# Performance work log

Measured on AMD Instinct MI355X. Metric: run time of the kernel, lower is better.

## Reference

```python
import jax, jax.numpy as jnp
import numpy as np

B, S, D, H = 4, 2048, 1024, 16
HD = D // H
MASKED_BIAS = -10000.0

def setup_inputs() -> dict:
    key = jax.random.key(0)
    ks = jax.random.split(key, 10)
    s = 0.02
    return {
        "hidden_states": jax.random.normal(ks[0], (B, S, D), dtype=jnp.float32),
        "Wq": jax.random.normal(ks[1], (D, D), dtype=jnp.float32) * s,
        "bq": jax.random.normal(ks[2], (D,), dtype=jnp.float32) * s,
        "Wk": jax.random.normal(ks[3], (D, D), dtype=jnp.float32) * s,
        "bk": jax.random.normal(ks[4], (D,), dtype=jnp.float32) * s,
        "Wv": jax.random.normal(ks[5], (D, D), dtype=jnp.float32) * s,
        "bv": jax.random.normal(ks[6], (D,), dtype=jnp.float32) * s,
        "Wo": jax.random.normal(ks[7], (D, D), dtype=jnp.float32) * s,
        "bo": jax.random.normal(ks[8], (D,), dtype=jnp.float32) * s,
        "comp": jnp.zeros((D,), dtype=jnp.float32),
    }

def reference(hidden_states, Wq, bq, Wk, bk, Wv, bv, Wo, bo, comp):
    x = hidden_states
    # torch Linear: y = x @ W.T + b
    q = (x @ Wq.T + bq).reshape(B, S, H, HD).transpose(0, 2, 1, 3)  # [B,H,S,hd]
    k = (x @ Wk.T + bk).reshape(B, S, H, HD).transpose(0, 2, 1, 3)
    v = (x @ Wv.T + bv).reshape(B, S, H, HD).transpose(0, 2, 1, 3)
    scores = jnp.einsum('bhqd,bhkd->bhqk', q, k) / jnp.sqrt(jnp.asarray(HD, dtype=q.dtype))
    causal = jnp.tril(jnp.ones((S, S), dtype=bool))  # [S,S]
    scores = jnp.where(causal[None, None], scores, jnp.asarray(MASKED_BIAS, dtype=scores.dtype))
    attn = jax.nn.softmax(scores, axis=-1)  # dropout p=0 (eval)
    out = jnp.einsum('bhqk,bhkd->bhqd', attn, v)  # [B,H,S,hd]
    out = out.transpose(0, 2, 1, 3).reshape(B, S, D)
    out = out @ Wo.T + bo
    out = out + comp[None, None, :]
    return out
```

## Files before the change

### kernel.cpp

```cpp
#include <hip/hip_runtime.h>
#include <hip/hip_bf16.h>

#define NB 4
#define NS 2048
#define ND 1024
#define NH 16
#define NHD 64
#define NM (NB*NS)

typedef __bf16 bf16_t;
typedef bf16_t bf8  __attribute__((ext_vector_type(8)));
typedef bf16_t bf4v __attribute__((ext_vector_type(4)));
typedef float  f4   __attribute__((ext_vector_type(4)));

#define GLDS16(g, l) __builtin_amdgcn_global_load_lds( \
    (const __attribute__((address_space(1))) void*)(g), \
    (__attribute__((address_space(3))) void*)(l), 16, 0, 0)

__global__ __launch_bounds__(256) void cvt_all(const float* __restrict__ x,
                                               const float* __restrict__ wq,
                                               const float* __restrict__ wk,
                                               const float* __restrict__ wv,
                                               const float* __restrict__ wo,
                                               bf16_t* __restrict__ Xb,
                                               bf16_t* __restrict__ Wqkv,
                                               bf16_t* __restrict__ Wob) {
    const int i = blockIdx.x * 256 + threadIdx.x;
    const float* src;
    bf16_t* dst;
    int off;
    if (i < 2097152) {
        src = x; dst = Xb; off = i;
    } else {
        const int j = i - 2097152;
        const int w = j >> 18;
        off = j & 262143;
        src = (w == 0 ? wq : w == 1 ? wk : w == 2 ? wv : wo);
        dst = (w == 3 ? Wob : Wqkv + ((size_t)w << 20));
    }
    const float4 v = ((const float4*)src)[off];
    bf4v o;
    o[0] = (bf16_t)v.x; o[1] = (bf16_t)v.y; o[2] = (bf16_t)v.z; o[3] = (bf16_t)v.w;
    ((bf4v*)dst)[off] = o;
}

__global__ __launch_bounds__(256) void gemm_qkv(const bf16_t* __restrict__ A,
                                                const bf16_t* __restrict__ Bw,
                                                const float* __restrict__ bq,
                                                const float* __restrict__ bk,
                                                const float* __restrict__ bv,
                                                bf16_t* __restrict__ Qh,
                                                bf16_t* __restrict__ Kh,
                                                bf16_t* __restrict__ VTh) {
    __shared__ __align__(16) bf16_t As[128 * 32];
    __shared__ __align__(16) bf16_t Bs[128 * 32];
    const int t = threadIdx.x;
    const int wave = t >> 6, lane = t & 63, ln = lane & 15, quad = lane >> 4;
    const int wm = (wave >> 1) * 64, wn = (wave & 1) * 64;
    const int m0 = blockIdx.y * 128, n0 = blockIdx.x * 128;
    const int K = 1024;

    f4 acc[4][4];
    const f4 z = {0.f, 0.f, 0.f, 0.f};
#pragma unroll
    for (int i = 0; i < 4; ++i)
#pragma unroll
        for (int j = 0; j < 4; ++j) acc[i][j] = z;

    const int srow = wave * 16 + (lane >> 2);
    const int scol = (lane & 3) * 8;
    const bf16_t* Ag0 = A  + (size_t)(m0 + srow) * K + scol;
    const bf16_t* Ag1 = A  + (size_t)(m0 + srow + 64) * K + scol;
    const bf16_t* Bg0 = Bw + (size_t)(n0 + srow) * K + scol;
    const bf16_t* Bg1 = Bw + (size_t)(n0 + srow + 64) * K + scol;
    bf16_t* Al0 = &As[srow * 32 + scol];
    bf16_t* Al1 = &As[(srow + 64) * 32 + scol];
    bf16_t* Bl0 = &Bs[srow * 32 + scol];
    bf16_t* Bl1 = &Bs[(srow + 64) * 32 + scol];

    for (int k0 = 0; k0 < K; k0 += 32) {
        __syncthreads();
        GLDS16(Ag0 + k0, Al0);
        GLDS16(Ag1 + k0, Al1);
        GLDS16(Bg0 + k0, Bl0);
        GLDS16(Bg1 + k0, Bl1);
        __syncthreads();
        bf8 af[4], bfr[4];
#pragma unroll
        for (int mt = 0; mt < 4; ++mt) af[mt]  = *(const bf8*)(&As[(wm + mt * 16 + ln) * 32 + quad * 8]);
#pragma unroll
        for (int nt = 0; nt < 4; ++nt) bfr[nt] = *(const bf8*)(&Bs[(wn + nt * 16 + ln) * 32 + quad * 8]);
#pragma unroll
        for (int mt = 0; mt < 4; ++mt)
#pragma unroll
            for (int nt = 0; nt < 4; ++nt)
                acc[mt][nt] = __builtin_amdgcn_mfma_f32_16x16x32_bf16(af[mt], bfr[nt], acc[mt][nt], 0, 0, 0);
    }

    const int sec = n0 >> 10;
#pragma unroll
    for (int nt = 0; nt < 4; ++nt) {
        const int gn = n0 + wn + nt * 16 + ln;
        const int nn = gn & 1023;
        const int hh = nn >> 6, d = nn & 63;
        const float bias = (sec == 0 ? bq[nn] : (sec == 1 ? bk[nn] : bv[nn]));
        if (sec < 2) {
            bf16_t* dstBase = (sec == 0 ? Qh : Kh);
#pragma unroll
            for (int mt = 0; mt < 4; ++mt) {
#pragma unroll
                for (int r = 0; r < 4; ++r) {
                    const int gm = m0 + wm + mt * 16 + quad * 4 + r;
                    const int b = gm >> 11, s = gm & 2047;
                    dstBase[((size_t)(b * NH + hh) * NS + s) * NHD + d] = (bf16_t)(acc[mt][nt][r] + bias);
                }
            }
        } else {
#pragma unroll
            for (int mt = 0; mt < 4; ++mt) {
                const int gm0 = m0 + wm + mt * 16 + quad * 4;
                const int b = gm0 >> 11, s = gm0 & 2047;
                bf4v pk;
#pragma unroll
                for (int r = 0; r < 4; ++r) pk[r] = (bf16_t)(acc[mt][nt][r] + bias);
                *(bf4v*)(&VTh[((size_t)(b * NH + hh) * NHD + d) * NS + s]) = pk;
            }
        }
    }
}

__global__ __launch_bounds__(256) void attn_kernel(const bf16_t* __restrict__ Q,
                                                   const bf16_t* __restrict__ K,
                                                   const bf16_t* __restrict__ VT,
                                                   bf16_t* __restrict__ O) {
    __shared__ __align__(16) bf16_t Ks[64 * 72];
    __shared__ __align__(16) bf16_t Vt[64 * 72];
    const int L = blockIdx.x;
    const int mm = L >> 3;
    const int h  = ((mm >> 5) << 3) | (L & 7);
    const int qt = 31 - (mm & 31);
    const int q0 = qt * 64;
    const int jmax = qt;
    const size_t head_off = (size_t)h * NS * NHD;
    const int t = threadIdx.x;
    const int wave = t >> 6, lane = t & 63, ln = lane & 15, quad = lane >> 4;

    const bf16_t* Qrow = Q + head_off + (size_t)(q0 + wave * 16 + ln) * NHD;
    bf8 qf0 = *(const bf8*)(Qrow + quad * 8);
    bf8 qf1 = *(const bf8*)(Qrow + 32 + quad * 8);
#pragma unroll
    for (int e = 0; e < 8; ++e) {
        qf0[e] = (bf16_t)((float)qf0[e] * 0.125f);
        qf1[e] = (bf16_t)((float)qf1[e] * 0.125f);
    }

    const bf16_t* Kg  = K  + head_off;
    const bf16_t* VTg = VT + head_off;
    const int krow0 = t >> 3, kcol = (t & 7) * 8;

    uint4 kr0 = *(const uint4*)(Kg + (size_t)krow0 * NHD + kcol);
    uint4 kr1 = *(const uint4*)(Kg + (size_t)(krow0 + 32) * NHD + kcol);
    uint4 vr0 = *(const uint4*)(VTg + (size_t)krow0 * NS + kcol);
    uint4 vr1 = *(const uint4*)(VTg + (size_t)(krow0 + 32) * NS + kcol);
    *(uint4*)(&Ks[krow0 * 72 + kcol])        = kr0;
    *(uint4*)(&Ks[(krow0 + 32) * 72 + kcol]) = kr1;
    *(uint4*)(&Vt[krow0 * 72 + kcol])        = vr0;
    *(uint4*)(&Vt[(krow0 + 32) * 72 + kcol]) = vr1;
    __syncthreads();

    f4 o[4];
    const f4 z = {0.f, 0.f, 0.f, 0.f};
#pragma unroll
    for (int i = 0; i < 4; ++i) o[i] = z;
    float ls = 0.f;

#pragma unroll 1
    for (int j = 0; j <= jmax; ++j) {
        if (j < jmax) {
            const size_t nb = (size_t)(j + 1) * 64;
            kr0 = *(const uint4*)(Kg + (nb + krow0) * NHD + kcol);
            kr1 = *(const uint4*)(Kg + (nb + krow0 + 32) * NHD + kcol);
            vr0 = *(const uint4*)(VTg + (size_t)krow0 * NS + nb + kcol);
            vr1 = *(const uint4*)(VTg + (size_t)(krow0 + 32) * NS + nb + kcol);
        }

        f4 s[4];
        __builtin_amdgcn_s_setprio(1);
#pragma unroll
        for (int nt = 0; nt < 4; ++nt) {
            const bf8 kf0 = *(const bf8*)(&Ks[(nt * 16 + ln) * 72 + quad * 8]);
            const bf8 kf1 = *(const bf8*)(&Ks[(nt * 16 + ln) * 72 + 32 + quad * 8]);
            s[nt] = z;
            s[nt] = __builtin_amdgcn_mfma_f32_16x16x32_bf16(kf0, qf0, s[nt], 0, 0, 0);
            s[nt] = __builtin_amdgcn_mfma_f32_16x16x32_bf16(kf1, qf1, s[nt], 0, 0, 0);
        }
        __builtin_amdgcn_s_setprio(0);

        if (j == jmax) {
            const int kv0 = j * 64;
            const int rowq = q0 + wave * 16 + ln;
#pragma unroll
            for (int nt = 0; nt < 4; ++nt) {
#pragma unroll
                for (int r = 0; r < 4; ++r)
                    if (kv0 + nt * 16 + quad * 4 + r > rowq) s[nt][r] = -1e30f;
            }
        }

#pragma unroll
        for (int nt = 0; nt < 4; ++nt)
#pragma unroll
            for (int r = 0; r < 4; ++r) {
                const float p = __expf(s[nt][r]);
                s[nt][r] = p;
                ls += p;
            }

        unsigned int w[4][2];
#pragma unroll
        for (int nt = 0; nt < 4; ++nt)
#pragma unroll
            for (int rr = 0; rr < 2; ++rr) {
                union { bf16_t hx[2]; unsigned int u; } u;
                u.hx[0] = (bf16_t)s[nt][2 * rr];
                u.hx[1] = (bf16_t)s[nt][2 * rr + 1];
                w[nt][rr] = u.u;
            }
        union Frag { unsigned int d[4]; bf8 v; } f0, f1;
        {
            unsigned int a, b;
            a = w[0][0]; b = w[1][0];
            asm volatile("v_permlane32_swap_b32 %0, %1" : "+v"(a), "+v"(b));
            asm volatile("v_permlane16_swap_b32 %0, %1" : "+v"(a), "+v"(b));
            f0.d[0] = a; f0.d[2] = b;
            a = w[0][1]; b = w[1][1];
            asm volatile("v_permlane32_swap_b32 %0, %1" : "+v"(a), "+v"(b));
            asm volatile("v_permlane16_swap_b32 %0, %1" : "+v"(a), "+v"(b));
            f0.d[1] = a; f0.d[3] = b;
            a = w[2][0]; b = w[3][0];
            asm volatile("v_permlane32_swap_b32 %0, %1" : "+v"(a), "+v"(b));
            asm volatile("v_permlane16_swap_b32 %0, %1" : "+v"(a), "+v"(b));
            f1.d[0] = a; f1.d[2] = b;
            a = w[2][1]; b = w[3][1];
            asm volatile("v_permlane32_swap_b32 %0, %1" : "+v"(a), "+v"(b));
            asm volatile("v_permlane16_swap_b32 %0, %1" : "+v"(a), "+v"(b));
            f1.d[1] = a; f1.d[3] = b;
        }
        const bf8 p0 = f0.v;
        const bf8 p1 = f1.v;

        __builtin_amdgcn_s_setprio(1);
#pragma unroll
        for (int dt = 0; dt < 4; ++dt) {
            const bf8 v0 = *(const bf8*)(&Vt[(dt * 16 + ln) * 72 + quad * 8]);
            const bf8 v1 = *(const bf8*)(&Vt[(dt * 16 + ln) * 72 + 32 + quad * 8]);
            o[dt] = __builtin_amdgcn_mfma_f32_16x16x32_bf16(p0, v0, o[dt], 0, 0, 0);
            o[dt] = __builtin_amdgcn_mfma_f32_16x16x32_bf16(p1, v1, o[dt], 0, 0, 0);
        }
        __builtin_amdgcn_s_setprio(0);

        if (j < jmax) {
            __syncthreads();
            *(uint4*)(&Ks[krow0 * 72 + kcol])        = kr0;
            *(uint4*)(&Ks[(krow0 + 32) * 72 + kcol]) = kr1;
            *(uint4*)(&Vt[krow0 * 72 + kcol])        = vr0;
            *(uint4*)(&Vt[(krow0 + 32) * 72 + kcol]) = vr1;
            __syncthreads();
        }
    }

    ls += __shfl_xor(ls, 16);
    ls += __shfl_xor(ls, 32);

    const int b = h >> 4, hh = h & 15;
#pragma unroll
    for (int r = 0; r < 4; ++r) {
        const float inv = 1.f / __shfl(ls, quad * 4 + r);
        const int gs = q0 + wave * 16 + quad * 4 + r;
#pragma unroll
        for (int dt = 0; dt < 4; ++dt)
            O[((size_t)(b * NS + gs)) * ND + hh * NHD + dt * 16 + ln] = (bf16_t)(o[dt][r] * inv);
    }
}

__global__ __launch_bounds__(256) void gemm_proj(const bf16_t* __restrict__ A,
                                                 const bf16_t* __restrict__ Bw,
                                                 const float* __restrict__ bo,
                                                 const float* __restrict__ comp,
                                                 float* __restrict__ out) {
    __shared__ __align__(16) bf16_t As[128 * 32];
    __shared__ __align__(16) bf16_t Bs[128 * 32];
    const int t = threadIdx.x;
    const int wave = t >> 6, lane = t & 63, ln = lane & 15, quad = lane >> 4;
    const int wm = (wave >> 1) * 64, wn = (wave & 1) * 64;
    const int nwg = gridDim.x * gridDim.y;
    int flat = blockIdx.y * gridDim.x + blockIdx.x;
    flat = (flat & 7) * (nwg >> 3) + (flat >> 3);
    const int m0 = (flat / gridDim.x) * 128, n0 = (flat % gridDim.x) * 128;
    const int K = 1024;

    f4 acc[4][4];
    const f4 z = {0.f, 0.f, 0.f, 0.f};
#pragma unroll
    for (int i = 0; i < 4; ++i)
#pragma unroll
        for (int j = 0; j < 4; ++j) acc[i][j] = z;

    const int srow = wave * 16 + (lane >> 2);
    const int scol = (lane & 3) * 8;
    const bf16_t* Ag0 = A  + (size_t)(m0 + srow) * K + scol;
    const bf16_t* Ag1 = A  + (size_t)(m0 + srow + 64) * K + scol;
    const bf16_t* Bg0 = Bw + (size_t)(n0 + srow) * K + scol;
    const bf16_t* Bg1 = Bw + (size_t)(n0 + srow + 64) * K + scol;
    bf16_t* Al0 = &As[srow * 32 + scol];
    bf16_t* Al1 = &As[(srow + 64) * 32 + scol];
    bf16_t* Bl0 = &Bs[srow * 32 + scol];
    bf16_t* Bl1 = &Bs[(srow + 64) * 32 + scol];

    for (int k0 = 0; k0 < K; k0 += 32) {
        __syncthreads();
        GLDS16(Ag0 + k0, Al0);
        GLDS16(Ag1 + k0, Al1);
        GLDS16(Bg0 + k0, Bl0);
        GLDS16(Bg1 + k0, Bl1);
        __syncthreads();
        bf8 af[4], bfr[4];
#pragma unroll
        for (int mt = 0; mt < 4; ++mt) af[mt]  = *(const bf8*)(&As[(wm + mt * 16 + ln) * 32 + quad * 8]);
#pragma unroll
        for (int nt = 0; nt < 4; ++nt) bfr[nt] = *(const bf8*)(&Bs[(wn + nt * 16 + ln) * 32 + quad * 8]);
#pragma unroll
        for (int mt = 0; mt < 4; ++mt)
#pragma unroll
            for (int nt = 0; nt < 4; ++nt)
                acc[mt][nt] = __builtin_amdgcn_mfma_f32_16x16x32_bf16(bfr[nt], af[mt], acc[mt][nt], 0, 0, 0);
    }

#pragma unroll
    for (int nt = 0; nt < 4; ++nt) {
        const int gn = n0 + wn + nt * 16 + quad * 4;
        const float4 b4 = *(const float4*)(bo + gn);
        const float4 c4 = *(const float4*)(comp + gn);
#pragma unroll
        for (int mt = 0; mt < 4; ++mt) {
            const int gm = m0 + wm + mt * 16 + ln;
            float4 v;
            v.x = acc[mt][nt][0] + b4.x + c4.x;
            v.y = acc[mt][nt][1] + b4.y + c4.y;
            v.z = acc[mt][nt][2] + b4.z + c4.z;
            v.w = acc[mt][nt][3] + b4.w + c4.w;
            *(float4*)(&out[(size_t)gm * ND + gn]) = v;
        }
    }
}

extern "C" void kernel_launch(void* const* d_in, const int* in_sizes, int n_in,
                              void* d_out, int out_size, void* d_ws, size_t ws_size,
                              hipStream_t stream) {
    const float* x    = (const float*)d_in[0];
    const float* Wq   = (const float*)d_in[1];
    const float* bq   = (const float*)d_in[2];
    const float* Wk   = (const float*)d_in[3];
    const float* bk   = (const float*)d_in[4];
    const float* Wv   = (const float*)d_in[5];
    const float* bv   = (const float*)d_in[6];
    const float* Wo   = (const float*)d_in[7];
    const float* bo   = (const float*)d_in[8];
    const float* comp = (const float*)d_in[9];
    float* out = (float*)d_out;

    char* w = (char*)d_ws;
    bf16_t* Xb   = (bf16_t*)(w);
    bf16_t* Wqkv = (bf16_t*)(w + 16777216);
    bf16_t* Wob  = (bf16_t*)(w + 23068672);
    bf16_t* Qh   = (bf16_t*)(w + 25165824);
    bf16_t* Kh   = (bf16_t*)(w + 41943040);
    bf16_t* VTh  = (bf16_t*)(w + 58720256);
    bf16_t* AOb  = (bf16_t*)(w + 75497472);

    cvt_all<<<12288, 256, 0, stream>>>(x, Wq, Wk, Wv, Wo, Xb, Wqkv, Wob);
    gemm_qkv<<<dim3(3072 / 128, NM / 128), 256, 0, stream>>>(Xb, Wqkv, bq, bk, bv, Qh, Kh, VTh);
    attn_kernel<<<2048, 256, 0, stream>>>(Qh, Kh, VTh, AOb);
    gemm_proj<<<dim3(1024 / 128, NM / 128), 256, 0, stream>>>(AOb, Wob, bo, comp, out);
}
```

Before: 273.5 us.

## Double-buffer LDS tiles in GEMMs and attention, swizzle QKV block order

Adds two-stage LDS buffering to both GEMM kernels and the attention kernel. The next K-slice (or K/V tile) is now issued into the alternate buffer while MFMAs run on the current one, which cuts each iteration from two barriers to one. The QKV GEMM also gets an XCD-style block remap (stride 192) to improve L2 locality. The cost is double the LDS per block, which may lower occupancy. The GEMM path also relies on the global_load_lds writes having completed at the single trailing barrier.

```diff
diff --git a/kernel.cpp b/kernel.cpp
--- a/kernel.cpp
+++ b/kernel.cpp
@@ -52,12 +52,14 @@
                                                 bf16_t* __restrict__ Qh,
                                                 bf16_t* __restrict__ Kh,
                                                 bf16_t* __restrict__ VTh) {
-    __shared__ __align__(16) bf16_t As[128 * 32];
-    __shared__ __align__(16) bf16_t Bs[128 * 32];
+    __shared__ __align__(16) bf16_t As[2][128 * 32];
+    __shared__ __align__(16) bf16_t Bs[2][128 * 32];
     const int t = threadIdx.x;
     const int wave = t >> 6, lane = t & 63, ln = lane & 15, quad = lane >> 4;
     const int wm = (wave >> 1) * 64, wn = (wave & 1) * 64;
-    const int m0 = blockIdx.y * 128, n0 = blockIdx.x * 128;
+    int flat = blockIdx.y * gridDim.x + blockIdx.x;
+    flat = (flat & 7) * 192 + (flat >> 3);
+    const int m0 = (flat / gridDim.x) * 128, n0 = (flat % gridDim.x) * 128;
     const int K = 1024;
 
     f4 acc[4][4];
@@ -73,28 +75,34 @@
     const bf16_t* Ag1 = A  + (size_t)(m0 + srow + 64) * K + scol;
     const bf16_t* Bg0 = Bw + (size_t)(n0 + srow) * K + scol;
     const bf16_t* Bg1 = Bw + (size_t)(n0 + srow + 64) * K + scol;
-    bf16_t* Al0 = &As[srow * 32 + scol];
-    bf16_t* Al1 = &As[(srow + 64) * 32 + scol];
-    bf16_t* Bl0 = &Bs[srow * 32 + scol];
-    bf16_t* Bl1 = &Bs[(srow + 64) * 32 + scol];
-
+    const int so0 = srow * 32 + scol, so1 = (srow + 64) * 32 + scol;
+
+    GLDS16(Ag0, &As[0][so0]);
+    GLDS16(Ag1, &As[0][so1]);
+    GLDS16(Bg0, &Bs[0][so0]);
+    GLDS16(Bg1, &Bs[0][so1]);
+    __syncthreads();
+
+    int cur = 0;
     for (int k0 = 0; k0 < K; k0 += 32) {
-        __syncthreads();
-        GLDS16(Ag0 + k0, Al0);
-        GLDS16(Ag1 + k0, Al1);
-        GLDS16(Bg0 + k0, Bl0);
-        GLDS16(Bg1 + k0, Bl1);
-        __syncthreads();
+        if (k0 + 32 < K) {
+            GLDS16(Ag0 + k0 + 32, &As[cur ^ 1][so0]);
+            GLDS16(Ag1 + k0 + 32, &As[cur ^ 1][so1]);
+            GLDS16(Bg0 + k0 + 32, &Bs[cur ^ 1][so0]);
+            GLDS16(Bg1 + k0 + 32, &Bs[cur ^ 1][so1]);
+        }
         bf8 af[4], bfr[4];
 #pragma unroll
-        for (int mt = 0; mt < 4; ++mt) af[mt]  = *(const bf8*)(&As[(wm + mt * 16 + ln) * 32 + quad * 8]);
-#pragma unroll
-        for (int nt = 0; nt < 4; ++nt) bfr[nt] = *(const bf8*)(&Bs[(wn + nt * 16 + ln) * 32 + quad * 8]);
+        for (int mt = 0; mt < 4; ++mt) af[mt]  = *(const bf8*)(&As[cur][(wm + mt * 16 + ln) * 32 + quad * 8]);
+#pragma unroll
+        for (int nt = 0; nt < 4; ++nt) bfr[nt] = *(const bf8*)(&Bs[cur][(wn + nt * 16 + ln) * 32 + quad * 8]);
 #pragma unroll
         for (int mt = 0; mt < 4; ++mt)
 #pragma unroll
             for (int nt = 0; nt < 4; ++nt)
                 acc[mt][nt] = __builtin_amdgcn_mfma_f32_16x16x32_bf16(af[mt], bfr[nt], acc[mt][nt], 0, 0, 0);
+        __syncthreads();
+        cur ^= 1;
     }
 
     const int sec = n0 >> 10;
@@ -133,8 +141,8 @@
                                                    const bf16_t* __restrict__ K,
                                                    const bf16_t* __restrict__ VT,
                                                    bf16_t* __restrict__ O) {
-    __shared__ __align__(16) bf16_t Ks[64 * 72];
-    __shared__ __align__(16) bf16_t Vt[64 * 72];
+    __shared__ __align__(16) bf16_t Ks[2][64 * 72];
+    __shared__ __align__(16) bf16_t Vt[2][64 * 72];
     const int L = blockIdx.x;
     const int mm = L >> 3;
     const int h  = ((mm >> 5) << 3) | (L & 7);
@@ -162,10 +170,10 @@
     uint4 kr1 = *(const uint4*)(Kg + (size_t)(krow0 + 32) * NHD + kcol);
     uint4 vr0 = *(const uint4*)(VTg + (size_t)krow0 * NS + kcol);
     uint4 vr1 = *(const uint4*)(VTg + (size_t)(krow0 + 32) * NS + kcol);
-    *(uint4*)(&Ks[krow0 * 72 + kcol])        = kr0;
-    *(uint4*)(&Ks[(krow0 + 32) * 72 + kcol]) = kr1;
-    *(uint4*)(&Vt[krow0 * 72 + kcol])        = vr0;
-    *(uint4*)(&Vt[(krow0 + 32) * 72 + kcol]) = vr1;
+    *(uint4*)(&Ks[0][krow0 * 72 + kcol])        = kr0;
+    *(uint4*)(&Ks[0][(krow0 + 32) * 72 + kcol]) = kr1;
+    *(uint4*)(&Vt[0][krow0 * 72 + kcol])        = vr0;
+    *(uint4*)(&Vt[0][(krow0 + 32) * 72 + kcol]) = vr1;
     __syncthreads();
 
     f4 o[4];
@@ -176,6 +184,8 @@
 
 #pragma unroll 1
     for (int j = 0; j <= jmax; ++j) {
+        const bf16_t* KsB = &Ks[j & 1][0];
+        const bf16_t* VtB = &Vt[j & 1][0];
         if (j < jmax) {
             const size_t nb = (size_t)(j + 1) * 64;
             kr0 = *(const uint4*)(Kg + (nb + krow0) * NHD + kcol);
@@ -188,8 +198,8 @@
         __builtin_amdgcn_s_setprio(1);
 #pragma unroll
         for (int nt = 0; nt < 4; ++nt) {
-            const bf8 kf0 = *(const bf8*)(&Ks[(nt * 16 + ln) * 72 + quad * 8]);
-            const bf8 kf1 = *(const bf8*)(&Ks[(nt * 16 + ln) * 72 + 32 + quad * 8]);
+            const bf8 kf0 = *(const bf8*)(&KsB[(nt * 16 + ln) * 72 + quad * 8]);
+            const bf8 kf1 = *(const bf8*)(&KsB[(nt * 16 + ln) * 72 + 32 + quad * 8]);
             s[nt] = z;
             s[nt] = __builtin_amdgcn_mfma_f32_16x16x32_bf16(kf0, qf0, s[nt], 0, 0, 0);
             s[nt] = __builtin_amdgcn_mfma_f32_16x16x32_bf16(kf1, qf1, s[nt], 0, 0, 0);
@@ -252,21 +262,22 @@
         __builtin_amdgcn_s_setprio(1);
 #pragma unroll
         for (int dt = 0; dt < 4; ++dt) {
-            const bf8 v0 = *(const bf8*)(&Vt[(dt * 16 + ln) * 72 + quad * 8]);
-            const bf8 v1 = *(const bf8*)(&Vt[(dt * 16 + ln) * 72 + 32 + quad * 8]);
+            const bf8 v0 = *(const bf8*)(&VtB[(dt * 16 + ln) * 72 + quad * 8]);
+            const bf8 v1 = *(const bf8*)(&VtB[(dt * 16 + ln) * 72 + 32 + quad * 8]);
             o[dt] = __builtin_amdgcn_mfma_f32_16x16x32_bf16(p0, v0, o[dt], 0, 0, 0);
             o[dt] = __builtin_amdgcn_mfma_f32_16x16x32_bf16(p1, v1, o[dt], 0, 0, 0);
         }
         __builtin_amdgcn_s_setprio(0);
 
         if (j < jmax) {
-            __syncthreads();
-            *(uint4*)(&Ks[krow0 * 72 + kcol])        = kr0;
-            *(uint4*)(&Ks[(krow0 + 32) * 72 + kcol]) = kr1;
-            *(uint4*)(&Vt[krow0 * 72 + kcol])        = vr0;
-            *(uint4*)(&Vt[(krow0 + 32) * 72 + kcol]) = vr1;
-            __syncthreads();
-        }
+            bf16_t* KsN = &Ks[(j + 1) & 1][0];
+            bf16_t* VtN = &Vt[(j + 1) & 1][0];
+            *(uint4*)(&KsN[krow0 * 72 + kcol])        = kr0;
+            *(uint4*)(&KsN[(krow0 + 32) * 72 + kcol]) = kr1;
+            *(uint4*)(&VtN[krow0 * 72 + kcol])        = vr0;
+            *(uint4*)(&VtN[(krow0 + 32) * 72 + kcol]) = vr1;
+        }
+        __syncthreads();
     }
 
     ls += __shfl_xor(ls, 16);
@@ -288,8 +299,8 @@
                                                  const float* __restrict__ bo,
                                                  const float* __restrict__ comp,
                                                  float* __restrict__ out) {
-    __shared__ __align__(16) bf16_t As[128 * 32];
-    __shared__ __align__(16) bf16_t Bs[128 * 32];
+    __shared__ __align__(16) bf16_t As[2][128 * 32];
+    __shared__ __align__(16) bf16_t Bs[2][128 * 32];
     const int t = threadIdx.x;
     const int wave = t >> 6, lane = t & 63, ln = lane & 15, quad = lane >> 4;
     const int wm = (wave >> 1) * 64, wn = (wave & 1) * 64;
@@ -312,28 +323,34 @@
     const bf16_t* Ag1 = A  + (size_t)(m0 + srow + 64) * K + scol;
     const bf16_t* Bg0 = Bw + (size_t)(n0 + srow) * K + scol;
     const bf16_t* Bg1 = Bw + (size_t)(n0 + srow + 64) * K + scol;
-    bf16_t* Al0 = &As[srow * 32 + scol];
-    bf16_t* Al1 = &As[(srow + 64) * 32 + scol];
-    bf16_t* Bl0 = &Bs[srow * 32 + scol];
-    bf16_t* Bl1 = &Bs[(srow + 64) * 32 + scol];
-
+    const int so0 = srow * 32 + scol, so1 = (srow + 64) * 32 + scol;
+
+    GLDS16(Ag0, &As[0][so0]);
+    GLDS16(Ag1, &As[0][so1]);
+    GLDS16(Bg0, &Bs[0][so0]);
+    GLDS16(Bg1, &Bs[0][so1]);
+    __syncthreads();
+
+    int cur = 0;
     for (int k0 = 0; k0 < K; k0 += 32) {
-        __syncthreads();
-        GLDS16(Ag0 + k0, Al0);
-        GLDS16(Ag1 + k0, Al1);
-        GLDS16(Bg0 + k0, Bl0);
-        GLDS16(Bg1 + k0, Bl1);
-        __syncthreads();
+        if (k0 + 32 < K) {
+            GLDS16(Ag0 + k0 + 32, &As[cur ^ 1][so0]);
+            GLDS16(Ag1 + k0 + 32, &As[cur ^ 1][so1]);
+            GLDS16(Bg0 + k0 + 32, &Bs[cur ^ 1][so0]);
+            GLDS16(Bg1 + k0 + 32, &Bs[cur ^ 1][so1]);
+        }
         bf8 af[4], bfr[4];
 #pragma unroll
-        for (int mt = 0; mt < 4; ++mt) af[mt]  = *(const bf8*)(&As[(wm + mt * 16 + ln) * 32 + quad * 8]);
-#pragma unroll
-        for (int nt = 0; nt < 4; ++nt) bfr[nt] = *(const bf8*)(&Bs[(wn + nt * 16 + ln) * 32 + quad * 8]);
+        for (int mt = 0; mt < 4; ++mt) af[mt]  = *(const bf8*)(&As[cur][(wm + mt * 16 + ln) * 32 + quad * 8]);
+#pragma unroll
+        for (int nt = 0; nt < 4; ++nt) bfr[nt] = *(const bf8*)(&Bs[cur][(wn + nt * 16 + ln) * 32 + quad * 8]);
 #pragma unroll
         for (int mt = 0; mt < 4; ++mt)
 #pragma unroll
             for (int nt = 0; nt < 4; ++nt)
                 acc[mt][nt] = __builtin_amdgcn_mfma_f32_16x16x32_bf16(bfr[nt], af[mt], acc[mt][nt], 0, 0, 0);
+        __syncthreads();
+        cur ^= 1;
     }
 
 #pragma unroll
```

New measurement: 282.3 us. +3.2%, slower.
